# Kernel tuning notes

Hardware: AMD Instinct MI355X
Metric: run time of the kernel (lower is better)

Reference implementation:

```python
import jax, jax.numpy as jnp
import numpy as np

SIGMA = 2.0
INF = 1.0e6
M, N, H, K, C_IN, C_OUT = 50000, 100000, 32, 15, 64, 64
RADIUS = 2.5


def setup_inputs() -> dict:
    key = jax.random.key(0)
    k1, k2, k3, k4, k5, k6 = jax.random.split(key, 6)
    q_points = jax.random.normal(k1, (M, 3), dtype=jnp.float32)
    s_points = jax.random.normal(k2, (N, 3), dtype=jnp.float32)
    s_feats = jax.random.normal(k3, (N, C_IN), dtype=jnp.float32)
    # index N refers to the padding point (placed at INF)
    neighbor_indices = jax.random.randint(k4, (M, H), 0, N + 1, dtype=jnp.int64)
    weights = jax.random.normal(k5, (K, C_IN, C_OUT), dtype=jnp.float32) * 0.05
    # kernel points inside sphere of RADIUS (stand-in for load_kernels buffer)
    kp = jax.random.normal(k6, (K, 3), dtype=jnp.float32)
    kp = kp / jnp.linalg.norm(kp, axis=1, keepdims=True) * RADIUS * 0.7
    kernel_points = kp.at[0].set(0.0)  # fixed='center'
    return {
        "q_points": q_points,
        "s_points": s_points,
        "s_feats": s_feats,
        "neighbor_indices": neighbor_indices,
        "weights": weights,
        "kernel_points": kernel_points,
    }


def reference(q_points, s_points, s_feats, neighbor_indices, weights, kernel_points):
    # pad support points with an 'infinity' shadow point at index N
    padded_pts = jnp.concatenate([s_points, jnp.full((1, 3), INF, s_points.dtype)], axis=0)
    neighbors = padded_pts[neighbor_indices]                    # (M, H, 3)
    rel = neighbors - q_points[:, None, :]                      # (M, H, 3)
    diff = rel[:, :, None, :] - kernel_points[None, None]       # (M, H, K, 3)
    sq_dist = jnp.sum(diff * diff, axis=-1)                     # (M, H, K)
    nbr_w = jnp.clip(1.0 - jnp.sqrt(sq_dist) / SIGMA, 0.0)      # (M, H, K)

    padded_feats = jnp.concatenate([s_feats, jnp.zeros((1, s_feats.shape[1]), s_feats.dtype)], axis=0)
    nbr_feats = padded_feats[neighbor_indices]                  # (M, H, C_in)

    weighted = jnp.einsum('mhk,mhc->mkc', nbr_w, nbr_feats)     # (M, K, C_in)
    out = jnp.einsum('mkc,kcd->md', weighted, weights)          # (M, C_out)

    # normalize by count of real (non-padding / nonzero-sum) neighbors
    nbr_sum = jnp.sum(nbr_feats, axis=-1)                       # (M, H)
    nbr_num = jnp.sum(nbr_sum > 0.0, axis=-1)                   # (M,)
    nbr_num = jnp.maximum(nbr_num, 1)
    return out / nbr_num[:, None].astype(out.dtype)
```

## Files before the change

kernel.cpp:

```cpp
#include <hip/hip_runtime.h>
#include <hip/hip_bf16.h>

#define MPTS 50000
#define NPTS 100000
#define KK 15
#define KC 1024
#define WTP 1036
#define STP 36

typedef __attribute__((ext_vector_type(8))) short short8;
typedef __attribute__((ext_vector_type(4))) short short4v;
typedef __attribute__((ext_vector_type(4))) float floatx4;

static __device__ __forceinline__ unsigned short f2bf(float f) {
    __hip_bfloat16 h = __float2bfloat16(f);
    return *reinterpret_cast<unsigned short*>(&h);
}

static __device__ __forceinline__ short8 lds_load8(const unsigned short* p) {
    const short4v a = *(const short4v*)p;
    const short4v b = *(const short4v*)(p + 4);
    short8 r;
    r[0] = a[0]; r[1] = a[1]; r[2] = a[2]; r[3] = a[3];
    r[4] = b[0]; r[5] = b[1]; r[6] = b[2]; r[7] = b[3];
    return r;
}

__global__ void prep_all(const float* __restrict__ sf, const float* __restrict__ w,
                         unsigned short* __restrict__ sfb, float* __restrict__ rs,
                         unsigned short* __restrict__ wbf2) {
    const int b = blockIdx.x, t = threadIdx.x;
    if (b < 6250) {
        const int i = b * 256 + t;
        const float4 v = *(const float4*)(sf + (size_t)i * 4);
        ushort4 o;
        o.x = f2bf(v.x); o.y = f2bf(v.y); o.z = f2bf(v.z); o.w = f2bf(v.w);
        *(ushort4*)(sfb + (size_t)i * 4) = o;
    } else if (b < 7032) {
        const int tt = (b - 6250) * 256 + t;
        const int row = tt >> 1, p = tt & 1;
        if (row < NPTS) {
            const float* base = sf + (size_t)row * 64 + p * 4;
            float4 r = *(const float4*)base;
#pragma unroll
            for (int i = 1; i < 8; i++) {
                const float4 x = *(const float4*)(base + i * 8);
                r.x += x.x; r.y += x.y; r.z += x.z; r.w += x.w;
            }
            float sp = (r.x + r.y) + (r.z + r.w);
            sp += __shfl_xor(sp, 1);
            if (p == 0) rs[row] = sp;
        }
    } else {
        const int e = (b - 7032) * 256 + t;
        const int lane = e & 63, s = (e >> 6) & 31, wq = e >> 11;
        const int d = wq * 16 + (lane & 15);
        const int lqp = lane >> 4;
        unsigned short o8[8];
#pragma unroll
        for (int j = 0; j < 8; j++) {
            const int kc = s * 32 + lqp * 8 + j;
            const int c = kc >> 4, k = kc & 15;
            o8[j] = (k < KK) ? f2bf(w[k * 4096 + c * 64 + d]) : (unsigned short)0;
        }
#pragma unroll
        for (int j = 0; j < 8; j++) wbf2[(size_t)e * 8 + j] = o8[j];
    }
}

__global__ __launch_bounds__(256, 3) void kpconv_fused(
    const float* __restrict__ q_points,
    const float* __restrict__ s_points,
    const unsigned short* __restrict__ sfb,
    const int*   __restrict__ nbr,
    const unsigned short* __restrict__ wbf2,
    const float* __restrict__ kpts,
    const float* __restrict__ rowsum,
    float* __restrict__ out)
{
    const int t    = threadIdx.x;
    const int m0   = blockIdx.x * 16;
    const int lane = t & 63;
    const int wv   = t >> 6;
    const int l15  = lane & 15;
    const int lq   = lane >> 4;

    __shared__ int idx_lds[16][32];
    __shared__ unsigned short stage[4][64 * STP];
    __shared__ unsigned short wtw[16 * WTP];

    {
        const int r = 4 * wv + lq;
        const int2 iv = *(const int2*)&nbr[(size_t)(m0 + r) * 32 + l15 * 2];
        *(int2*)&idx_lds[r][l15 * 2] = iv;
    }

    ushort4 g[4][8];
    const int c4 = l15 * 4;
#pragma unroll
    for (int mi = 0; mi < 4; mi++) {
        const int m = 4 * wv + mi;
#pragma unroll
        for (int g2 = 0; g2 < 4; g2++) {
            const int r0 = g2 * 8 + lq * 2;
            const int2 ip = *(const int2*)&idx_lds[m][r0];
            g[mi][2 * g2]     = (ip.x < NPTS) ? *(const ushort4*)&sfb[(size_t)ip.x * 64 + c4]
                                              : make_ushort4(0, 0, 0, 0);
            g[mi][2 * g2 + 1] = (ip.y < NPTS) ? *(const ushort4*)&sfb[(size_t)ip.y * 64 + c4]
                                              : make_ushort4(0, 0, 0, 0);
        }
    }

    float inv[4];
#pragma unroll
    for (int s = 0; s < 2; s++) {
        const int m = 4 * wv + 2 * s + (lane >> 5);
        const int h = lane & 31;
        const int idx = idx_lds[m][h];
        float px = 1.0e6f, py = 1.0e6f, pz = 1.0e6f;
        if (idx < NPTS) {
            px = s_points[idx * 3 + 0];
            py = s_points[idx * 3 + 1];
            pz = s_points[idx * 3 + 2];
        }
        const float rx = px - q_points[(m0 + m) * 3 + 0];
        const float ry = py - q_points[(m0 + m) * 3 + 1];
        const float rz = pz - q_points[(m0 + m) * 3 + 2];
        unsigned short* wrow = &wtw[m * WTP];
#pragma unroll
        for (int k = 0; k < KK; k++) {
            const float dx = rx - kpts[k * 3 + 0];
            const float dy = ry - kpts[k * 3 + 1];
            const float dz = rz - kpts[k * 3 + 2];
            const float d2 = dx * dx + dy * dy + dz * dz;
            wrow[k * STP + h] = f2bf(fmaxf(1.0f - sqrtf(d2) * 0.5f, 0.0f));
        }
        wrow[15 * STP + h] = 0;

        const bool ok = (idx < NPTS) && (rowsum[idx] > 0.0f);
        const unsigned long long bal = __ballot(ok);
        const int cLo = __popc((unsigned)bal);
        const int cHi = __popc((unsigned)(bal >> 32));
        inv[2 * s + 0] = 1.0f / (float)(cLo < 1 ? 1 : cLo);
        inv[2 * s + 1] = 1.0f / (float)(cHi < 1 ? 1 : cHi);
    }

    unsigned short* const st = stage[wv];
    const int swzw = (l15 >> 2) << 2;
#pragma unroll
    for (int mi = 0; mi < 4; mi++) {
        const int m = 4 * wv + mi;

#pragma unroll
        for (int g2 = 0; g2 < 4; g2++) {
            const int so = (((g2 * 4 + lq) ^ swzw)) * 2;
            const ushort4 a = g[mi][2 * g2];
            const ushort4 b = g[mi][2 * g2 + 1];
            *(unsigned*)&st[(c4 + 0) * STP + so] = (unsigned)a.x | ((unsigned)b.x << 16);
            *(unsigned*)&st[(c4 + 1) * STP + so] = (unsigned)a.y | ((unsigned)b.y << 16);
            *(unsigned*)&st[(c4 + 2) * STP + so] = (unsigned)a.z | ((unsigned)b.z << 16);
            *(unsigned*)&st[(c4 + 3) * STP + so] = (unsigned)a.w | ((unsigned)b.w << 16);
        }

        const short8 afrag = lds_load8(&wtw[m * WTP + l15 * STP + lq * 8]);
        const float iv = inv[mi];
#pragma unroll
        for (int ct = 0; ct < 4; ct++) {
            const short8 bfrag = lds_load8(&st[(ct * 16 + l15) * STP + ((lq ^ ct) * 8)]);
            floatx4 d = {0.f, 0.f, 0.f, 0.f};
            d = __builtin_amdgcn_mfma_f32_16x16x32_bf16(afrag, bfrag, d, 0, 0, 0);
            ushort4 pk;
            pk.x = f2bf(d[0] * iv);
            pk.y = f2bf(d[1] * iv);
            pk.z = f2bf(d[2] * iv);
            pk.w = f2bf(d[3] * iv);
            *(ushort4*)&wtw[m * WTP + (ct * 16 + l15) * 16 + lq * 4] = pk;
        }
    }
    __syncthreads();

    {
        floatx4 acc = {0.f, 0.f, 0.f, 0.f};
        const unsigned short* ap = &wtw[l15 * WTP + lq * 8];
        const unsigned short* bp = wbf2 + ((size_t)(wv * 32) * 64 + lane) * 8;
#pragma unroll 8
        for (int s = 0; s < 32; s++) {
            const short8 a = lds_load8(ap + s * 32);
            const short8 b = *(const short8*)(bp + s * 512);
            acc = __builtin_amdgcn_mfma_f32_16x16x32_bf16(a, b, acc, 0, 0, 0);
        }
        const int d = wv * 16 + l15;
#pragma unroll
        for (int r = 0; r < 4; r++)
            out[(size_t)(m0 + lq * 4 + r) * 64 + d] = acc[r];
    }
}

extern "C" void kernel_launch(void* const* d_in, const int* in_sizes, int n_in,
                              void* d_out, int out_size, void* d_ws, size_t ws_size,
                              hipStream_t stream) {
    const float* q_points = (const float*)d_in[0];
    const float* s_points = (const float*)d_in[1];
    const float* s_feats  = (const float*)d_in[2];
    const int*   nbr      = (const int*)d_in[3];
    const float* weights  = (const float*)d_in[4];
    const float* kpts     = (const float*)d_in[5];
    float* out = (float*)d_out;

    char* ws = (char*)d_ws;
    unsigned short* wbf2 = (unsigned short*)ws;
    float* rowsum = (float*)(ws + 131072);
    unsigned short* sfb = (unsigned short*)(ws + 532480);

    prep_all<<<7064, 256, 0, stream>>>(s_feats, weights, sfb, rowsum, wbf2);
    kpconv_fused<<<MPTS / 16, 256, 0, stream>>>(q_points, s_points, sfb, nbr,
                                                wbf2, kpts, rowsum, out);
}
```

Baseline: 150.5 us.

## Halve query tile per block, fuse bf16 convert with rowsum, precompute kernel-point terms

The prep kernel now converts features to bf16 in the same pass that computes row sums, and adds a zero padding row plus a precomputed kernel-point table (-2*kp, |kp|^2). The main kernel handles 8 query points per block instead of 16, raises the occupancy hint to 4 blocks per SM, and applies normalization at the final output store. This frees registers for more parallelism and removes the separate conversion pass, but half the lanes of the second MFMA stage do redundant work and each block reloads the full weight matrix, doubling weight traffic. Distances use the expanded-square form with a clamp, which can differ slightly in rounding.

```diff
diff --git a/kernel.cpp b/kernel.cpp
--- a/kernel.cpp
+++ b/kernel.cpp
@@ -4,7 +4,7 @@
 #define MPTS 50000
 #define NPTS 100000
 #define KK 15
-#define KC 1024
+#define TM 8
 #define WTP 1036
 #define STP 36
 
@@ -27,32 +27,35 @@
 }
 
 __global__ void prep_all(const float* __restrict__ sf, const float* __restrict__ w,
+                         const float* __restrict__ kpts,
                          unsigned short* __restrict__ sfb, float* __restrict__ rs,
-                         unsigned short* __restrict__ wbf2) {
+                         unsigned short* __restrict__ wbf2, float4* __restrict__ kpp) {
     const int b = blockIdx.x, t = threadIdx.x;
-    if (b < 6250) {
-        const int i = b * 256 + t;
-        const float4 v = *(const float4*)(sf + (size_t)i * 4);
-        ushort4 o;
-        o.x = f2bf(v.x); o.y = f2bf(v.y); o.z = f2bf(v.z); o.w = f2bf(v.w);
-        *(ushort4*)(sfb + (size_t)i * 4) = o;
-    } else if (b < 7032) {
-        const int tt = (b - 6250) * 256 + t;
+    if (b < 782) {
+        const int tt = b * 256 + t;
         const int row = tt >> 1, p = tt & 1;
         if (row < NPTS) {
             const float* base = sf + (size_t)row * 64 + p * 4;
             float4 r = *(const float4*)base;
+            {
+                ushort4 o;
+                o.x = f2bf(r.x); o.y = f2bf(r.y); o.z = f2bf(r.z); o.w = f2bf(r.w);
+                *(ushort4*)&sfb[(size_t)row * 64 + p * 4] = o;
+            }
 #pragma unroll
             for (int i = 1; i < 8; i++) {
                 const float4 x = *(const float4*)(base + i * 8);
+                ushort4 o;
+                o.x = f2bf(x.x); o.y = f2bf(x.y); o.z = f2bf(x.z); o.w = f2bf(x.w);
+                *(ushort4*)&sfb[(size_t)row * 64 + i * 8 + p * 4] = o;
                 r.x += x.x; r.y += x.y; r.z += x.z; r.w += x.w;
             }
             float sp = (r.x + r.y) + (r.z + r.w);
             sp += __shfl_xor(sp, 1);
             if (p == 0) rs[row] = sp;
         }
-    } else {
-        const int e = (b - 7032) * 256 + t;
+    } else if (b < 814) {
+        const int e = (b - 782) * 256 + t;
         const int lane = e & 63, s = (e >> 6) & 31, wq = e >> 11;
         const int d = wq * 16 + (lane & 15);
         const int lqp = lane >> 4;
@@ -65,95 +68,102 @@
         }
 #pragma unroll
         for (int j = 0; j < 8; j++) wbf2[(size_t)e * 8 + j] = o8[j];
-    }
-}
-
-__global__ __launch_bounds__(256, 3) void kpconv_fused(
+    } else {
+        if (t < 16) *(ushort4*)&sfb[(size_t)NPTS * 64 + t * 4] = make_ushort4(0, 0, 0, 0);
+        else if (t == 16) rs[NPTS] = -1.0f;
+        else if (t >= 32 && t < 32 + KK) {
+            const int k = t - 32;
+            const float kx = kpts[k * 3 + 0], ky = kpts[k * 3 + 1], kz = kpts[k * 3 + 2];
+            kpp[k] = make_float4(-2.f * kx, -2.f * ky, -2.f * kz, kx * kx + ky * ky + kz * kz);
+        }
+    }
+}
+
+__global__ __launch_bounds__(256, 4) void kpconv_fused(
     const float* __restrict__ q_points,
     const float* __restrict__ s_points,
     const unsigned short* __restrict__ sfb,
     const int*   __restrict__ nbr,
     const unsigned short* __restrict__ wbf2,
-    const float* __restrict__ kpts,
+    const float4* __restrict__ kpp,
     const float* __restrict__ rowsum,
     float* __restrict__ out)
 {
     const int t    = threadIdx.x;
-    const int m0   = blockIdx.x * 16;
+    const int m0   = blockIdx.x * TM;
     const int lane = t & 63;
     const int wv   = t >> 6;
     const int l15  = lane & 15;
     const int lq   = lane >> 4;
 
-    __shared__ int idx_lds[16][32];
+    __shared__ int idx_lds[TM][32];
     __shared__ unsigned short stage[4][64 * STP];
-    __shared__ unsigned short wtw[16 * WTP];
-
-    {
-        const int r = 4 * wv + lq;
-        const int2 iv = *(const int2*)&nbr[(size_t)(m0 + r) * 32 + l15 * 2];
-        *(int2*)&idx_lds[r][l15 * 2] = iv;
-    }
-
-    ushort4 g[4][8];
+    __shared__ unsigned short wtw[TM * WTP];
+    __shared__ float inv_lds[TM];
+
+    const int mw = 2 * wv + (lane >> 5);
+    const int h  = lane & 31;
+    idx_lds[mw][h] = nbr[(size_t)(m0 + mw) * 32 + h];
+
+    ushort4 g[2][8];
     const int c4 = l15 * 4;
 #pragma unroll
-    for (int mi = 0; mi < 4; mi++) {
-        const int m = 4 * wv + mi;
+    for (int mi = 0; mi < 2; mi++) {
+        const int m = 2 * wv + mi;
 #pragma unroll
         for (int g2 = 0; g2 < 4; g2++) {
             const int r0 = g2 * 8 + lq * 2;
             const int2 ip = *(const int2*)&idx_lds[m][r0];
-            g[mi][2 * g2]     = (ip.x < NPTS) ? *(const ushort4*)&sfb[(size_t)ip.x * 64 + c4]
-                                              : make_ushort4(0, 0, 0, 0);
-            g[mi][2 * g2 + 1] = (ip.y < NPTS) ? *(const ushort4*)&sfb[(size_t)ip.y * 64 + c4]
-                                              : make_ushort4(0, 0, 0, 0);
-        }
-    }
-
-    float inv[4];
-#pragma unroll
-    for (int s = 0; s < 2; s++) {
-        const int m = 4 * wv + 2 * s + (lane >> 5);
-        const int h = lane & 31;
-        const int idx = idx_lds[m][h];
+            const int i0 = min(ip.x, NPTS);
+            const int i1 = min(ip.y, NPTS);
+            g[mi][2 * g2]     = *(const ushort4*)&sfb[(size_t)i0 * 64 + c4];
+            g[mi][2 * g2 + 1] = *(const ushort4*)&sfb[(size_t)i1 * 64 + c4];
+        }
+    }
+
+    {
+        const int idx = idx_lds[mw][h];
         float px = 1.0e6f, py = 1.0e6f, pz = 1.0e6f;
         if (idx < NPTS) {
             px = s_points[idx * 3 + 0];
             py = s_points[idx * 3 + 1];
             pz = s_points[idx * 3 + 2];
         }
-        const float rx = px - q_points[(m0 + m) * 3 + 0];
-        const float ry = py - q_points[(m0 + m) * 3 + 1];
-        const float rz = pz - q_points[(m0 + m) * 3 + 2];
-        unsigned short* wrow = &wtw[m * WTP];
+        const float rx = px - q_points[(m0 + mw) * 3 + 0];
+        const float ry = py - q_points[(m0 + mw) * 3 + 1];
+        const float rz = pz - q_points[(m0 + mw) * 3 + 2];
+        const float r2 = rx * rx + ry * ry + rz * rz;
+        unsigned short* wrow = &wtw[mw * WTP];
 #pragma unroll
         for (int k = 0; k < KK; k++) {
-            const float dx = rx - kpts[k * 3 + 0];
-            const float dy = ry - kpts[k * 3 + 1];
-            const float dz = rz - kpts[k * 3 + 2];
-            const float d2 = dx * dx + dy * dy + dz * dz;
-            wrow[k * STP + h] = f2bf(fmaxf(1.0f - sqrtf(d2) * 0.5f, 0.0f));
+            const float4 kp = kpp[k];
+            float d2 = kp.w;
+            d2 = fmaf(rx, kp.x, d2);
+            d2 = fmaf(ry, kp.y, d2);
+            d2 = fmaf(rz, kp.z, d2);
+            d2 = fmaxf(r2 + d2, 0.0f);
+            const float wv_ = fmaxf(fmaf(-0.5f, __builtin_amdgcn_sqrtf(d2), 1.0f), 0.0f);
+            wrow[k * STP + h] = f2bf(wv_);
         }
         wrow[15 * STP + h] = 0;
 
-        const bool ok = (idx < NPTS) && (rowsum[idx] > 0.0f);
+        const bool ok = rowsum[min(idx, NPTS)] > 0.0f;
         const unsigned long long bal = __ballot(ok);
-        const int cLo = __popc((unsigned)bal);
-        const int cHi = __popc((unsigned)(bal >> 32));
-        inv[2 * s + 0] = 1.0f / (float)(cLo < 1 ? 1 : cLo);
-        inv[2 * s + 1] = 1.0f / (float)(cHi < 1 ? 1 : cHi);
+        if (h == 0) {
+            const int cnt = __popc((unsigned)(bal >> ((lane >> 5) * 32)));
+            inv_lds[mw] = 1.0f / (float)(cnt < 1 ? 1 : cnt);
+        }
     }
 
     unsigned short* const st = stage[wv];
     const int swzw = (l15 >> 2) << 2;
 #pragma unroll
-    for (int mi = 0; mi < 4; mi++) {
-        const int m = 4 * wv + mi;
+    for (int mi = 0; mi < 2; mi++) {
+        const int m = 2 * wv + mi;
 
 #pragma unroll
         for (int g2 = 0; g2 < 4; g2++) {
-            const int so = (((g2 * 4 + lq) ^ swzw)) * 2;
+            const int so = ((g2 * 4 + lq) ^ swzw) * 2;
             const ushort4 a = g[mi][2 * g2];
             const ushort4 b = g[mi][2 * g2 + 1];
             *(unsigned*)&st[(c4 + 0) * STP + so] = (unsigned)a.x | ((unsigned)b.x << 16);
@@ -163,17 +173,13 @@
         }
 
         const short8 afrag = lds_load8(&wtw[m * WTP + l15 * STP + lq * 8]);
-        const float iv = inv[mi];
 #pragma unroll
         for (int ct = 0; ct < 4; ct++) {
             const short8 bfrag = lds_load8(&st[(ct * 16 + l15) * STP + ((lq ^ ct) * 8)]);
             floatx4 d = {0.f, 0.f, 0.f, 0.f};
             d = __builtin_amdgcn_mfma_f32_16x16x32_bf16(afrag, bfrag, d, 0, 0, 0);
             ushort4 pk;
-            pk.x = f2bf(d[0] * iv);
-            pk.y = f2bf(d[1] * iv);
-            pk.z = f2bf(d[2] * iv);
-            pk.w = f2bf(d[3] * iv);
+            pk.x = f2bf(d[0]); pk.y = f2bf(d[1]); pk.z = f2bf(d[2]); pk.w = f2bf(d[3]);
             *(ushort4*)&wtw[m * WTP + (ct * 16 + l15) * 16 + lq * 4] = pk;
         }
     }
@@ -181,7 +187,7 @@
 
     {
         floatx4 acc = {0.f, 0.f, 0.f, 0.f};
-        const unsigned short* ap = &wtw[l15 * WTP + lq * 8];
+        const unsigned short* ap = &wtw[(l15 & 7) * WTP + lq * 8];
         const unsigned short* bp = wbf2 + ((size_t)(wv * 32) * 64 + lane) * 8;
 #pragma unroll 8
         for (int s = 0; s < 32; s++) {
@@ -189,10 +195,14 @@
             const short8 b = *(const short8*)(bp + s * 512);
             acc = __builtin_amdgcn_mfma_f32_16x16x32_bf16(a, b, acc, 0, 0, 0);
         }
-        const int d = wv * 16 + l15;
-#pragma unroll
-        for (int r = 0; r < 4; r++)
-            out[(size_t)(m0 + lq * 4 + r) * 64 + d] = acc[r];
+        if (lq < 2) {
+            const int d = wv * 16 + l15;
+#pragma unroll
+            for (int r = 0; r < 4; r++) {
+                const int m = lq * 4 + r;
+                out[(size_t)(m0 + m) * 64 + d] = acc[r] * inv_lds[m];
+            }
+        }
     }
 }
 
@@ -210,9 +220,10 @@
     char* ws = (char*)d_ws;
     unsigned short* wbf2 = (unsigned short*)ws;
     float* rowsum = (float*)(ws + 131072);
+    float4* kpp = (float4*)(ws + 531600);
     unsigned short* sfb = (unsigned short*)(ws + 532480);
 
-    prep_all<<<7064, 256, 0, stream>>>(s_feats, weights, sfb, rowsum, wbf2);
-    kpconv_fused<<<MPTS / 16, 256, 0, stream>>>(q_points, s_points, sfb, nbr,
-                                                wbf2, kpts, rowsum, out);
-}
+    prep_all<<<815, 256, 0, stream>>>(s_feats, weights, kpts, sfb, rowsum, wbf2, kpp);
+    kpconv_fused<<<MPTS / TM, 256, 0, stream>>>(q_points, s_points, sfb, nbr,
+                                                wbf2, kpp, rowsum, out);
+}
```

Result: no change. 149.2 us (-0.9%).
